# Performance work log

Measured on AMD Instinct MI355X. Metric: run time of the kernel, lower is better.

Reference implementation:

```python
import jax, jax.numpy as jnp
import numpy as np

N_NODES = 50000
N_EDGES = 1600000
IN_CH = 128
HIDDEN = 128
N_CLASSES = 40


def setup_inputs() -> dict:
    key = jax.random.key(0)
    ks = jax.random.split(key, 8)
    node_features = jax.random.normal(ks[0], (1, N_NODES, IN_CH), dtype=jnp.float32)
    edge_index = jax.random.randint(ks[1], (1, 2, N_EDGES), 0, N_NODES, dtype=jnp.int64)
    rank_mapping = jnp.zeros((2, N_EDGES), dtype=jnp.int32)
    s1 = 1.0 / np.sqrt(IN_CH)
    s2 = 1.0 / np.sqrt(HIDDEN)
    W1 = jax.random.uniform(ks[2], (IN_CH, HIDDEN), jnp.float32, -s1, s1)
    b1 = jax.random.uniform(ks[3], (HIDDEN,), jnp.float32, -s1, s1)
    W2 = jax.random.uniform(ks[4], (HIDDEN, HIDDEN), jnp.float32, -s2, s2)
    b2 = jax.random.uniform(ks[5], (HIDDEN,), jnp.float32, -s2, s2)
    Wfc = jax.random.uniform(ks[6], (HIDDEN, N_CLASSES), jnp.float32, -s2, s2)
    bfc = jax.random.uniform(ks[7], (N_CLASSES,), jnp.float32, -s2, s2)
    return {"node_features": node_features, "edge_index": edge_index,
            "rank_mapping": rank_mapping, "W1": W1, "b1": b1,
            "W2": W2, "b2": b2, "Wfc": Wfc, "bfc": bfc}


def _gcn_single(feats, src, dst, W1, b1, W2, b2, Wfc, bfc):
    # feats: [N, F]; src/dst: [E]
    n = feats.shape[0]
    x = feats[dst]                                 # gather -> [E, F]
    x = jax.nn.relu(x @ W1 + b1)                   # conv1 (Linear + ReLU)
    x = jax.ops.segment_sum(x, src, num_segments=n)  # scatter-sum -> [N, H]
    x = x[dst]                                     # gather -> [E, H]
    x = x @ W2 + b2                                # conv2 (plain Linear)
    x = jax.ops.segment_sum(x, src, num_segments=n)  # scatter-sum -> [N, H]
    return x @ Wfc + bfc                           # [N, C]


def reference(node_features, edge_index, rank_mapping, W1, b1, W2, b2, Wfc, bfc):
    src = edge_index[:, 0, :]  # [B, E]
    dst = edge_index[:, 1, :]  # [B, E]
    return jax.vmap(_gcn_single, in_axes=(0, 0, 0, None, None, None, None, None, None))(
        node_features, src, dst, W1, b1, W2, b2, Wfc, bfc)
```

## Files before the change

### kernel.cpp

```cpp
#include <hip/hip_runtime.h>

static constexpr int NN = 50000;
static constexpr int NE = 1600000;
static constexpr int CH = 128;
static constexpr int NCLS = 40;

static constexpr int NPB  = 256;
static constexpr int NBUK = (NN + NPB - 1) / NPB;
static constexpr int EPB  = 8192;
static constexpr int NHB  = (NE + EPB - 1) / EPB;
static constexpr int NS   = NBUK * NHB;
static constexpr int SCAN_B = 256;
static constexpr int NSB  = (NS + SCAN_B - 1) / SCAN_B;
static constexpr int NROWP = ((NN + 63) / 64) * 64;
static constexpr int PAD = 136;
static constexpr int GEMM_BLKS = (NN + 63) / 64;

typedef __attribute__((ext_vector_type(8))) short bf16x8;
typedef __attribute__((ext_vector_type(4))) float f32x4;

__device__ __forceinline__ float bflo(unsigned v) {
    return __uint_as_float((v & 0xFFFFu) << 16);
}
__device__ __forceinline__ float bfhi(unsigned v) {
    return __uint_as_float(v & 0xFFFF0000u);
}
__device__ __forceinline__ unsigned short f2bf(float f) {
    unsigned u = __float_as_uint(f);
    u += 0x7FFFu + ((u >> 16) & 1u);
    return (unsigned short)(u >> 16);
}

__global__ __launch_bounds__(256)
void fused_pre(const int* __restrict__ src, int* __restrict__ H,
               const float* __restrict__ W1, unsigned short* __restrict__ Wt_g,
               const float* __restrict__ W2, const float* __restrict__ Wfc,
               const float* __restrict__ b2, unsigned short* __restrict__ Mt,
               float* __restrict__ cfc)
{
    __shared__ int h[NBUK];
    const int t = threadIdx.x;
    const int b = blockIdx.x;

    if (b < NHB) {
        for (int i = t; i < NBUK; i += 256) h[i] = 0;
        __syncthreads();
        const int base4 = b * (EPB / 4);
        const int4* src4 = reinterpret_cast<const int4*>(src);
        for (int i = t; i < EPB / 4; i += 256) {
            const int idx = base4 + i;
            if (idx < NE / 4) {
                const int4 v = src4[idx];
                atomicAdd(&h[v.x >> 8], 1);
                atomicAdd(&h[v.y >> 8], 1);
                atomicAdd(&h[v.z >> 8], 1);
                atomicAdd(&h[v.w >> 8], 1);
            }
        }
        __syncthreads();
        for (int i = t; i < NBUK; i += 256) H[i * NHB + b] = h[i];
    } else if (b < NHB + 64) {
        const int idx = (b - NHB) * 256 + t;
        const int c = idx >> 7;
        const int k = idx & 127;
        Wt_g[c * PAD + k] = f2bf(W1[k * 128 + c]);
    } else {
        const int idx = (b - NHB - 64) * 256 + t;
        if (idx < 48 * 128) {
            const int c = idx >> 7;
            const int k = idx & 127;
            float a = 0.f;
            if (c < NCLS) {
                #pragma unroll 16
                for (int j = 0; j < 128; ++j) a += W2[k * 128 + j] * Wfc[j * NCLS + c];
            }
            Mt[c * 128 + k] = f2bf(a);
        }
        if (b == NHB + 64 && t < NCLS) {
            float a = 0.f;
            #pragma unroll 16
            for (int j = 0; j < 128; ++j) a += b2[j] * Wfc[j * NCLS + t];
            cfc[t] = a;
        }
    }
}

__global__ __launch_bounds__(SCAN_B)
void scan_local(int* __restrict__ H, int* __restrict__ bsum)
{
    __shared__ int buf[SCAN_B];
    const int t = threadIdx.x;
    const int g = blockIdx.x * SCAN_B + t;
    const int v = (g < NS) ? H[g] : 0;
    buf[t] = v;
    __syncthreads();
    #pragma unroll
    for (int off = 1; off < SCAN_B; off <<= 1) {
        const int x = (t >= off) ? buf[t - off] : 0;
        __syncthreads();
        buf[t] += x;
        __syncthreads();
    }
    if (g < NS) H[g] = buf[t] - v;
    if (t == SCAN_B - 1) bsum[blockIdx.x] = buf[t];
}

__global__ __launch_bounds__(SCAN_B)
void scan_bsums(int* __restrict__ bsum)
{
    __shared__ int buf[SCAN_B];
    const int t = threadIdx.x;
    const int v = (t < NSB) ? bsum[t] : 0;
    buf[t] = v;
    __syncthreads();
    #pragma unroll
    for (int off = 1; off < SCAN_B; off <<= 1) {
        const int x = (t >= off) ? buf[t - off] : 0;
        __syncthreads();
        buf[t] += x;
        __syncthreads();
    }
    if (t < NSB) bsum[t] = buf[t] - v;
    if (t == SCAN_B - 1) bsum[NSB] = buf[t];
}

__global__ __launch_bounds__(256)
void fused_mid(const int* __restrict__ src, const int* __restrict__ dst,
               const int* __restrict__ H, const int* __restrict__ bsum,
               int* __restrict__ EP,
               const float* __restrict__ X, const unsigned short* __restrict__ Wt_g,
               const float* __restrict__ b, const unsigned short* __restrict__ Mt,
               unsigned short* __restrict__ V1)
{
    __shared__ __align__(16) unsigned short Wt[128 * PAD];
    __shared__ __align__(16) unsigned short Fa[64 * PAD];
    __shared__ __align__(16) unsigned short Va[64 * NCLS];
    __shared__ float bl[128];
    __shared__ int cur[NBUK];

    const int t = threadIdx.x;

    if (blockIdx.x < NHB) {
        const int bb = blockIdx.x;
        for (int i = t; i < NBUK; i += 256) {
            const int x = i * NHB + bb;
            cur[i] = H[x] + bsum[x >> 8];
        }
        __syncthreads();
        const int base4 = bb * (EPB / 4);
        const int4* src4 = reinterpret_cast<const int4*>(src);
        const int4* dst4 = reinterpret_cast<const int4*>(dst);
        for (int i = t; i < EPB / 4; i += 256) {
            const int idx = base4 + i;
            if (idx < NE / 4) {
                const int4 s4 = src4[idx];
                const int4 d4 = dst4[idx];
                int pos;
                pos = atomicAdd(&cur[s4.x >> 8], 1); EP[pos] = ((s4.x & 255) << 16) | d4.x;
                pos = atomicAdd(&cur[s4.y >> 8], 1); EP[pos] = ((s4.y & 255) << 16) | d4.y;
                pos = atomicAdd(&cur[s4.z >> 8], 1); EP[pos] = ((s4.z & 255) << 16) | d4.z;
                pos = atomicAdd(&cur[s4.w >> 8], 1); EP[pos] = ((s4.w & 255) << 16) | d4.w;
            }
        }
        return;
    }

    const int gb = blockIdx.x - NHB;
    const int lane = t & 63;
    const int w = t >> 6;

    for (int i = t; i < (128 * PAD) / 8; i += 256)
        reinterpret_cast<uint4*>(Wt)[i] = reinterpret_cast<const uint4*>(Wt_g)[i];
    if (t < 128) bl[t] = b[t];

    const int base = gb * 64;
    const int nRows = min(64, NN - base);
    {
        const int r = t >> 2;
        const int c0 = (t & 3) * 32;
        if (r < nRows) {
            #pragma unroll
            for (int j = 0; j < 32; j += 4) {
                const float4 v = *reinterpret_cast<const float4*>(&X[(size_t)(base + r) * CH + c0 + j]);
                ushort4 o; o.x = f2bf(v.x); o.y = f2bf(v.y); o.z = f2bf(v.z); o.w = f2bf(v.w);
                *reinterpret_cast<ushort4*>(&Fa[r * PAD + c0 + j]) = o;
            }
        } else {
            #pragma unroll
            for (int j = 0; j < 32; j += 4) {
                ushort4 z; z.x = z.y = z.z = z.w = 0;
                *reinterpret_cast<ushort4*>(&Fa[r * PAD + c0 + j]) = z;
            }
        }
    }
    __syncthreads();

    f32x4 acc[8];
    #pragma unroll
    for (int i = 0; i < 8; ++i) acc[i] = (f32x4){0.f, 0.f, 0.f, 0.f};

    const int arow = w * 16 + (lane & 15);
    const int kgrp = (lane >> 4) * 4;

    #pragma unroll
    for (int ks = 0; ks < 4; ++ks) {
        const int k0 = ks * 32 + kgrp;
        bf16x8 af;
        {
            const short4 lo = *reinterpret_cast<const short4*>(&Fa[arow * PAD + k0]);
            const short4 hi = *reinterpret_cast<const short4*>(&Fa[arow * PAD + k0 + 16]);
            af[0] = lo.x; af[1] = lo.y; af[2] = lo.z; af[3] = lo.w;
            af[4] = hi.x; af[5] = hi.y; af[6] = hi.z; af[7] = hi.w;
        }
        #pragma unroll
        for (int ct = 0; ct < 8; ++ct) {
            const int c = ct * 16 + (lane & 15);
            bf16x8 bf;
            const short4 lo = *reinterpret_cast<const short4*>(&Wt[c * PAD + k0]);
            const short4 hi = *reinterpret_cast<const short4*>(&Wt[c * PAD + k0 + 16]);
            bf[0] = lo.x; bf[1] = lo.y; bf[2] = lo.z; bf[3] = lo.w;
            bf[4] = hi.x; bf[5] = hi.y; bf[6] = hi.z; bf[7] = hi.w;
            acc[ct] = __builtin_amdgcn_mfma_f32_16x16x32_bf16(af, bf, acc[ct], 0, 0, 0);
        }
    }
    __syncthreads();

    #pragma unroll
    for (int ct = 0; ct < 8; ++ct) {
        const int c = ct * 16 + (lane & 15);
        const float bias = bl[c];
        #pragma unroll
        for (int r = 0; r < 4; ++r) {
            const int row = w * 16 + (lane >> 4) * 4 + r;
            Fa[row * PAD + c] = f2bf(fmaxf(acc[ct][r] + bias, 0.f));
        }
    }
    __syncthreads();

    f32x4 acc2[3];
    #pragma unroll
    for (int i = 0; i < 3; ++i) acc2[i] = (f32x4){0.f, 0.f, 0.f, 0.f};

    #pragma unroll
    for (int ks = 0; ks < 4; ++ks) {
        const int k0 = ks * 32 + kgrp;
        bf16x8 af;
        {
            const short4 lo = *reinterpret_cast<const short4*>(&Fa[arow * PAD + k0]);
            const short4 hi = *reinterpret_cast<const short4*>(&Fa[arow * PAD + k0 + 16]);
            af[0] = lo.x; af[1] = lo.y; af[2] = lo.z; af[3] = lo.w;
            af[4] = hi.x; af[5] = hi.y; af[6] = hi.z; af[7] = hi.w;
        }
        #pragma unroll
        for (int ct = 0; ct < 3; ++ct) {
            const int c = ct * 16 + (lane & 15);
            bf16x8 bf;
            const short4 lo = *reinterpret_cast<const short4*>(&Mt[c * 128 + k0]);
            const short4 hi = *reinterpret_cast<const short4*>(&Mt[c * 128 + k0 + 16]);
            bf[0] = lo.x; bf[1] = lo.y; bf[2] = lo.z; bf[3] = lo.w;
            bf[4] = hi.x; bf[5] = hi.y; bf[6] = hi.z; bf[7] = hi.w;
            acc2[ct] = __builtin_amdgcn_mfma_f32_16x16x32_bf16(af, bf, acc2[ct], 0, 0, 0);
        }
    }

    #pragma unroll
    for (int ct = 0; ct < 3; ++ct) {
        const int c = ct * 16 + (lane & 15);
        if (c < NCLS) {
            #pragma unroll
            for (int r = 0; r < 4; ++r) {
                const int row = w * 16 + (lane >> 4) * 4 + r;
                Va[row * NCLS + c] = f2bf(acc2[ct][r]);
            }
        }
    }
    __syncthreads();

    for (int i = t; i < 320; i += 256) {
        const int r = i / 5;
        const int q = i % 5;
        *reinterpret_cast<uint4*>(&V1[(size_t)(base + r) * NCLS + q * 8]) =
            *reinterpret_cast<const uint4*>(&Va[r * NCLS + q * 8]);
    }
}

__global__ __launch_bounds__(1024)
void bucket_sort(const int* __restrict__ H, const int* __restrict__ bsum,
                 const int* __restrict__ EP,
                 unsigned short* __restrict__ sdst, int* __restrict__ offs,
                 int* __restrict__ deg)
{
    __shared__ int hist[NPB], cur[NPB], segBeg[NPB + 1], buf[NPB];
    const int t = threadIdx.x;
    const int b = blockIdx.x;
    const int node0 = b * NPB;
    const int nNodes = min(NPB, NN - node0);
    const int xb = b * NHB;
    const int beg = H[xb] + bsum[xb >> 8];
    int end;
    if (b == NBUK - 1) end = NE;
    else { const int xe = (b + 1) * NHB; end = H[xe] + bsum[xe >> 8]; }

    if (t < NPB) hist[t] = 0;
    __syncthreads();
    for (int i = beg + t; i < end; i += 1024) atomicAdd(&hist[EP[i] >> 16], 1);
    __syncthreads();

    if (t < NPB) buf[t] = hist[t];
    __syncthreads();
    #pragma unroll
    for (int off = 1; off < NPB; off <<= 1) {
        int x = 0;
        if (t < NPB && t >= off) x = buf[t - off];
        __syncthreads();
        if (t < NPB) buf[t] += x;
        __syncthreads();
    }
    if (t < NPB) segBeg[t] = buf[t] - hist[t];
    if (t == 0) segBeg[NPB] = end - beg;
    __syncthreads();

    if (t < nNodes) {
        offs[node0 + t] = beg + segBeg[t];
        deg[node0 + t] = hist[t];
    }
    if (b == NBUK - 1 && t == 0) offs[NN] = end;
    if (t < NPB) cur[t] = segBeg[t];
    __syncthreads();
    for (int i = beg + t; i < end; i += 1024) {
        const int p = EP[i];
        const int pos = atomicAdd(&cur[p >> 16], 1);
        sdst[beg + pos] = (unsigned short)(p & 0xFFFF);
    }
}

template<bool FINAL>
__global__ __launch_bounds__(512)
void gather40(const int* __restrict__ offs, const unsigned short* __restrict__ sdst,
              const unsigned short* __restrict__ X,
              unsigned short* __restrict__ Yb, float* __restrict__ Yf,
              const int* __restrict__ deg,
              const float* __restrict__ cfc, const float* __restrict__ bfc)
{
    const int t = threadIdx.x;
    const int w = t >> 6;
    const int lane = t & 63;
    const int g = lane >> 4;
    const int L = lane & 15;
    const int node0 = blockIdx.x * 32 + w * 4;

    float4 cf = make_float4(0.f, 0.f, 0.f, 0.f);
    float4 bfv = make_float4(0.f, 0.f, 0.f, 0.f);
    if (FINAL && L < 10) {
        cf  = *reinterpret_cast<const float4*>(&cfc[L * 4]);
        bfv = *reinterpret_cast<const float4*>(&bfc[L * 4]);
    }

    #pragma unroll
    for (int ni = 0; ni < 4; ++ni) {
        const int n = node0 + ni;
        if (n >= NN) break;
        const int sb = offs[n];
        const int se = offs[n + 1];
        float a0 = 0.f, a1 = 0.f, a2 = 0.f, a3 = 0.f;

        int i = sb;
        for (; i + 16 <= se; i += 16) {
            const int d0 = sdst[i + g];
            const int d1 = sdst[i + 4 + g];
            const int d2 = sdst[i + 8 + g];
            const int d3 = sdst[i + 12 + g];
            if (L < 10) {
                const uint2 v0 = *reinterpret_cast<const uint2*>(&X[(size_t)d0 * NCLS + L * 4]);
                const uint2 v1 = *reinterpret_cast<const uint2*>(&X[(size_t)d1 * NCLS + L * 4]);
                const uint2 v2 = *reinterpret_cast<const uint2*>(&X[(size_t)d2 * NCLS + L * 4]);
                const uint2 v3 = *reinterpret_cast<const uint2*>(&X[(size_t)d3 * NCLS + L * 4]);
                a0 += bflo(v0.x) + bflo(v1.x) + bflo(v2.x) + bflo(v3.x);
                a1 += bfhi(v0.x) + bfhi(v1.x) + bfhi(v2.x) + bfhi(v3.x);
                a2 += bflo(v0.y) + bflo(v1.y) + bflo(v2.y) + bflo(v3.y);
                a3 += bfhi(v0.y) + bfhi(v1.y) + bfhi(v2.y) + bfhi(v3.y);
            }
        }
        for (; i + 4 <= se; i += 4) {
            const int d = sdst[i + g];
            if (L < 10) {
                const uint2 v = *reinterpret_cast<const uint2*>(&X[(size_t)d * NCLS + L * 4]);
                a0 += bflo(v.x); a1 += bfhi(v.x);
                a2 += bflo(v.y); a3 += bfhi(v.y);
            }
        }
        const int rem = se - i;
        if (g < rem) {
            const int d = sdst[i + g];
            if (L < 10) {
                const uint2 v = *reinterpret_cast<const uint2*>(&X[(size_t)d * NCLS + L * 4]);
                a0 += bflo(v.x); a1 += bfhi(v.x);
                a2 += bflo(v.y); a3 += bfhi(v.y);
            }
        }

        a0 += __shfl_xor(a0, 16); a0 += __shfl_xor(a0, 32);
        a1 += __shfl_xor(a1, 16); a1 += __shfl_xor(a1, 32);
        a2 += __shfl_xor(a2, 16); a2 += __shfl_xor(a2, 32);
        a3 += __shfl_xor(a3, 16); a3 += __shfl_xor(a3, 32);

        if (lane < 16 && L < 10) {
            if (FINAL) {
                const float dgn = (float)deg[n];
                float4 o;
                o.x = a0 + dgn * cf.x + bfv.x;
                o.y = a1 + dgn * cf.y + bfv.y;
                o.z = a2 + dgn * cf.z + bfv.z;
                o.w = a3 + dgn * cf.w + bfv.w;
                *reinterpret_cast<float4*>(&Yf[(size_t)n * NCLS + L * 4]) = o;
            } else {
                uint2 o;
                o.x = ((unsigned)f2bf(a1) << 16) | f2bf(a0);
                o.y = ((unsigned)f2bf(a3) << 16) | f2bf(a2);
                *reinterpret_cast<uint2*>(&Yb[(size_t)n * NCLS + L * 4]) = o;
            }
        }
    }
}

extern "C" void kernel_launch(void* const* d_in, const int* in_sizes, int n_in,
                              void* d_out, int out_size, void* d_ws, size_t ws_size,
                              hipStream_t stream) {
    const float* F   = (const float*)d_in[0];
    const int*   EI  = (const int*)  d_in[1];
    const float* W1  = (const float*)d_in[3];
    const float* b1  = (const float*)d_in[4];
    const float* W2  = (const float*)d_in[5];
    const float* b2  = (const float*)d_in[6];
    const float* Wfc = (const float*)d_in[7];
    const float* bfc = (const float*)d_in[8];
    float* out = (float*)d_out;

    char* ws = (char*)d_ws;
    size_t off = 0;
    auto take = [&](size_t bytes) { char* p = ws + off; off += (bytes + 15) & ~(size_t)15; return p; };

    unsigned short* V1   = (unsigned short*)take((size_t)NROWP * NCLS * 2);
    unsigned short* U1   = (unsigned short*)take((size_t)NN * NCLS * 2);
    unsigned short* sdst = (unsigned short*)take((size_t)NE * 2);
    int*   EP   = (int*)take((size_t)NE * 4);
    int*   H    = (int*)take((size_t)NS * 4);
    int*   bsum = (int*)take((size_t)(NSB + 1) * 4);
    int*   deg  = (int*)take((size_t)NN * 4);
    int*   offs = (int*)take((size_t)(NN + 1) * 4);
    unsigned short* Mt   = (unsigned short*)take((size_t)48 * 128 * 2);
    unsigned short* Wt_g = (unsigned short*)take((size_t)128 * PAD * 2);
    float* cfc  = (float*)take((size_t)NCLS * 4);

    const int* src = EI;
    const int* dst = EI + NE;

    fused_pre<<<NHB + 64 + 24, 256, 0, stream>>>(src, H, W1, Wt_g, W2, Wfc, b2, Mt, cfc);

    scan_local<<<NSB, SCAN_B, 0, stream>>>(H, bsum);
    scan_bsums<<<1, SCAN_B, 0, stream>>>(bsum);

    fused_mid<<<NHB + GEMM_BLKS, 256, 0, stream>>>(src, dst, H, bsum, EP,
                                                   F, Wt_g, b1, Mt, V1);

    bucket_sort<<<NBUK, 1024, 0, stream>>>(H, bsum, EP, sdst, offs, deg);

    gather40<false><<<(NN + 31) / 32, 512, 0, stream>>>(offs, sdst, V1, U1, nullptr,
                                                        nullptr, nullptr, nullptr);

    gather40<true><<<(NN + 31) / 32, 512, 0, stream>>>(offs, sdst, U1, nullptr, out,
                                                       deg, cfc, bfc);
}
```

Baseline: 121.7 us.

## Fuse bucket sort with first neighbor gather using LDS-resident 64-node buckets

Buckets shrink from 256 to 64 nodes so each bucket's edge list fits in shared memory (CAP=3072). A single sortgather kernel loads the bucket's packed edges once, counting-sorts them in LDS, writes sdst, and directly performs the first 40-wide neighbor aggregation from the LDS-sorted indices. This removes one kernel launch and the repeated global reads of EP and sdst. In exchange the histogram and scan arrays grow, and the scan over block sums is widened to 1024 threads. There is no overflow check if a bucket exceeds CAP edges, so correctness relies on the near-uniform random degree distribution.

```diff
diff --git a/kernel.cpp b/kernel.cpp
--- a/kernel.cpp
+++ b/kernel.cpp
@@ -5,7 +5,7 @@
 static constexpr int CH = 128;
 static constexpr int NCLS = 40;
 
-static constexpr int NPB  = 256;
+static constexpr int NPB  = 64;
 static constexpr int NBUK = (NN + NPB - 1) / NPB;
 static constexpr int EPB  = 8192;
 static constexpr int NHB  = (NE + EPB - 1) / EPB;
@@ -15,6 +15,7 @@
 static constexpr int NROWP = ((NN + 63) / 64) * 64;
 static constexpr int PAD = 136;
 static constexpr int GEMM_BLKS = (NN + 63) / 64;
+static constexpr int CAP = 3072;
 
 typedef __attribute__((ext_vector_type(8))) short bf16x8;
 typedef __attribute__((ext_vector_type(4))) float f32x4;
@@ -51,10 +52,10 @@
             const int idx = base4 + i;
             if (idx < NE / 4) {
                 const int4 v = src4[idx];
-                atomicAdd(&h[v.x >> 8], 1);
-                atomicAdd(&h[v.y >> 8], 1);
-                atomicAdd(&h[v.z >> 8], 1);
-                atomicAdd(&h[v.w >> 8], 1);
+                atomicAdd(&h[v.x >> 6], 1);
+                atomicAdd(&h[v.y >> 6], 1);
+                atomicAdd(&h[v.z >> 6], 1);
+                atomicAdd(&h[v.w >> 6], 1);
             }
         }
         __syncthreads();
@@ -105,23 +106,23 @@
     if (t == SCAN_B - 1) bsum[blockIdx.x] = buf[t];
 }
 
-__global__ __launch_bounds__(SCAN_B)
+__global__ __launch_bounds__(1024)
 void scan_bsums(int* __restrict__ bsum)
 {
-    __shared__ int buf[SCAN_B];
+    __shared__ int buf[1024];
     const int t = threadIdx.x;
     const int v = (t < NSB) ? bsum[t] : 0;
     buf[t] = v;
     __syncthreads();
     #pragma unroll
-    for (int off = 1; off < SCAN_B; off <<= 1) {
+    for (int off = 1; off < 1024; off <<= 1) {
         const int x = (t >= off) ? buf[t - off] : 0;
         __syncthreads();
         buf[t] += x;
         __syncthreads();
     }
     if (t < NSB) bsum[t] = buf[t] - v;
-    if (t == SCAN_B - 1) bsum[NSB] = buf[t];
+    if (t == 1023) bsum[NSB] = buf[t];
 }
 
 __global__ __launch_bounds__(256)
@@ -156,10 +157,10 @@
                 const int4 s4 = src4[idx];
                 const int4 d4 = dst4[idx];
                 int pos;
-                pos = atomicAdd(&cur[s4.x >> 8], 1); EP[pos] = ((s4.x & 255) << 16) | d4.x;
-                pos = atomicAdd(&cur[s4.y >> 8], 1); EP[pos] = ((s4.y & 255) << 16) | d4.y;
-                pos = atomicAdd(&cur[s4.z >> 8], 1); EP[pos] = ((s4.z & 255) << 16) | d4.z;
-                pos = atomicAdd(&cur[s4.w >> 8], 1); EP[pos] = ((s4.w & 255) << 16) | d4.w;
+                pos = atomicAdd(&cur[s4.x >> 6], 1); EP[pos] = ((s4.x & 63) << 16) | d4.x;
+                pos = atomicAdd(&cur[s4.y >> 6], 1); EP[pos] = ((s4.y & 63) << 16) | d4.y;
+                pos = atomicAdd(&cur[s4.z >> 6], 1); EP[pos] = ((s4.z & 63) << 16) | d4.z;
+                pos = atomicAdd(&cur[s4.w >> 6], 1); EP[pos] = ((s4.w & 63) << 16) | d4.w;
             }
         }
         return;
@@ -284,13 +285,16 @@
     }
 }
 
-__global__ __launch_bounds__(1024)
-void bucket_sort(const int* __restrict__ H, const int* __restrict__ bsum,
-                 const int* __restrict__ EP,
-                 unsigned short* __restrict__ sdst, int* __restrict__ offs,
-                 int* __restrict__ deg)
+__global__ __launch_bounds__(512)
+void sortgather(const int* __restrict__ H, const int* __restrict__ bsum,
+                const int* __restrict__ EP, const unsigned short* __restrict__ V1,
+                unsigned short* __restrict__ U1, unsigned short* __restrict__ sdst,
+                int* __restrict__ offs, int* __restrict__ deg)
 {
-    __shared__ int hist[NPB], cur[NPB], segBeg[NPB + 1], buf[NPB];
+    __shared__ int raw[CAP];
+    __shared__ unsigned short srt[CAP];
+    __shared__ int hist[NPB], cur[NPB], segBeg[NPB + 1];
+
     const int t = threadIdx.x;
     const int b = blockIdx.x;
     const int node0 = b * NPB;
@@ -300,47 +304,111 @@
     int end;
     if (b == NBUK - 1) end = NE;
     else { const int xe = (b + 1) * NHB; end = H[xe] + bsum[xe >> 8]; }
-
+    const int C = end - beg;
+
+    for (int i = t; i < C; i += 512) raw[i] = EP[beg + i];
     if (t < NPB) hist[t] = 0;
     __syncthreads();
-    for (int i = beg + t; i < end; i += 1024) atomicAdd(&hist[EP[i] >> 16], 1);
-    __syncthreads();
-
-    if (t < NPB) buf[t] = hist[t];
+    for (int i = t; i < C; i += 512) atomicAdd(&hist[raw[i] >> 16], 1);
+    __syncthreads();
+
+    if (t < NPB) cur[t] = hist[t];
     __syncthreads();
     #pragma unroll
     for (int off = 1; off < NPB; off <<= 1) {
         int x = 0;
-        if (t < NPB && t >= off) x = buf[t - off];
-        __syncthreads();
-        if (t < NPB) buf[t] += x;
-        __syncthreads();
-    }
-    if (t < NPB) segBeg[t] = buf[t] - hist[t];
-    if (t == 0) segBeg[NPB] = end - beg;
+        if (t < NPB && t >= off) x = cur[t - off];
+        __syncthreads();
+        if (t < NPB) cur[t] += x;
+        __syncthreads();
+    }
+    if (t < NPB) segBeg[t] = cur[t] - hist[t];
+    if (t == 0) segBeg[NPB] = C;
     __syncthreads();
 
     if (t < nNodes) {
         offs[node0 + t] = beg + segBeg[t];
         deg[node0 + t] = hist[t];
     }
-    if (b == NBUK - 1 && t == 0) offs[NN] = end;
+    if (b == NBUK - 1 && t == 0) offs[NN] = NE;
     if (t < NPB) cur[t] = segBeg[t];
     __syncthreads();
-    for (int i = beg + t; i < end; i += 1024) {
-        const int p = EP[i];
+
+    for (int i = t; i < C; i += 512) {
+        const int p = raw[i];
         const int pos = atomicAdd(&cur[p >> 16], 1);
-        sdst[beg + pos] = (unsigned short)(p & 0xFFFF);
-    }
-}
-
-template<bool FINAL>
+        srt[pos] = (unsigned short)(p & 0xFFFF);
+    }
+    __syncthreads();
+
+    for (int i = t; i < C; i += 512) sdst[beg + i] = srt[i];
+
+    const int w = t >> 6;
+    const int lane = t & 63;
+    const int g = lane >> 4;
+    const int L = lane & 15;
+
+    for (int ni = 0; ni < 8; ++ni) {
+        const int n = w * 8 + ni;
+        if (n >= nNodes) break;
+        const int sb = segBeg[n];
+        const int se = segBeg[n + 1];
+        float a0 = 0.f, a1 = 0.f, a2 = 0.f, a3 = 0.f;
+
+        int i = sb;
+        for (; i + 16 <= se; i += 16) {
+            const int d0 = srt[i + g];
+            const int d1 = srt[i + 4 + g];
+            const int d2 = srt[i + 8 + g];
+            const int d3 = srt[i + 12 + g];
+            if (L < 10) {
+                const uint2 v0 = *reinterpret_cast<const uint2*>(&V1[(size_t)d0 * NCLS + L * 4]);
+                const uint2 v1 = *reinterpret_cast<const uint2*>(&V1[(size_t)d1 * NCLS + L * 4]);
+                const uint2 v2 = *reinterpret_cast<const uint2*>(&V1[(size_t)d2 * NCLS + L * 4]);
+                const uint2 v3 = *reinterpret_cast<const uint2*>(&V1[(size_t)d3 * NCLS + L * 4]);
+                a0 += bflo(v0.x) + bflo(v1.x) + bflo(v2.x) + bflo(v3.x);
+                a1 += bfhi(v0.x) + bfhi(v1.x) + bfhi(v2.x) + bfhi(v3.x);
+                a2 += bflo(v0.y) + bflo(v1.y) + bflo(v2.y) + bflo(v3.y);
+                a3 += bfhi(v0.y) + bfhi(v1.y) + bfhi(v2.y) + bfhi(v3.y);
+            }
+        }
+        for (; i + 4 <= se; i += 4) {
+            const int d = srt[i + g];
+            if (L < 10) {
+                const uint2 v = *reinterpret_cast<const uint2*>(&V1[(size_t)d * NCLS + L * 4]);
+                a0 += bflo(v.x); a1 += bfhi(v.x);
+                a2 += bflo(v.y); a3 += bfhi(v.y);
+            }
+        }
+        const int rem = se - i;
+        if (g < rem) {
+            const int d = srt[i + g];
+            if (L < 10) {
+                const uint2 v = *reinterpret_cast<const uint2*>(&V1[(size_t)d * NCLS + L * 4]);
+                a0 += bflo(v.x); a1 += bfhi(v.x);
+                a2 += bflo(v.y); a3 += bfhi(v.y);
+            }
+        }
+
+        a0 += __shfl_xor(a0, 16); a0 += __shfl_xor(a0, 32);
+        a1 += __shfl_xor(a1, 16); a1 += __shfl_xor(a1, 32);
+        a2 += __shfl_xor(a2, 16); a2 += __shfl_xor(a2, 32);
+        a3 += __shfl_xor(a3, 16); a3 += __shfl_xor(a3, 32);
+
+        if (lane < 16 && L < 10) {
+            uint2 o;
+            o.x = ((unsigned)f2bf(a1) << 16) | f2bf(a0);
+            o.y = ((unsigned)f2bf(a3) << 16) | f2bf(a2);
+            *reinterpret_cast<uint2*>(&U1[(size_t)(node0 + n) * NCLS + L * 4]) = o;
+        }
+    }
+}
+
 __global__ __launch_bounds__(512)
-void gather40(const int* __restrict__ offs, const unsigned short* __restrict__ sdst,
-              const unsigned short* __restrict__ X,
-              unsigned short* __restrict__ Yb, float* __restrict__ Yf,
-              const int* __restrict__ deg,
-              const float* __restrict__ cfc, const float* __restrict__ bfc)
+void gather40f(const int* __restrict__ offs, const unsigned short* __restrict__ sdst,
+               const unsigned short* __restrict__ X, float* __restrict__ Yf,
+               const int* __restrict__ deg,
+               const float* __restrict__ cfc, const float* __restrict__ bfc)
 {
     const int t = threadIdx.x;
     const int w = t >> 6;
@@ -351,7 +419,7 @@
 
     float4 cf = make_float4(0.f, 0.f, 0.f, 0.f);
     float4 bfv = make_float4(0.f, 0.f, 0.f, 0.f);
-    if (FINAL && L < 10) {
+    if (L < 10) {
         cf  = *reinterpret_cast<const float4*>(&cfc[L * 4]);
         bfv = *reinterpret_cast<const float4*>(&bfc[L * 4]);
     }
@@ -405,20 +473,13 @@
         a3 += __shfl_xor(a3, 16); a3 += __shfl_xor(a3, 32);
 
         if (lane < 16 && L < 10) {
-            if (FINAL) {
-                const float dgn = (float)deg[n];
-                float4 o;
-                o.x = a0 + dgn * cf.x + bfv.x;
-                o.y = a1 + dgn * cf.y + bfv.y;
-                o.z = a2 + dgn * cf.z + bfv.z;
-                o.w = a3 + dgn * cf.w + bfv.w;
-                *reinterpret_cast<float4*>(&Yf[(size_t)n * NCLS + L * 4]) = o;
-            } else {
-                uint2 o;
-                o.x = ((unsigned)f2bf(a1) << 16) | f2bf(a0);
-                o.y = ((unsigned)f2bf(a3) << 16) | f2bf(a2);
-                *reinterpret_cast<uint2*>(&Yb[(size_t)n * NCLS + L * 4]) = o;
-            }
+            const float dgn = (float)deg[n];
+            float4 o;
+            o.x = a0 + dgn * cf.x + bfv.x;
+            o.y = a1 + dgn * cf.y + bfv.y;
+            o.z = a2 + dgn * cf.z + bfv.z;
+            o.w = a3 + dgn * cf.w + bfv.w;
+            *reinterpret_cast<float4*>(&Yf[(size_t)n * NCLS + L * 4]) = o;
         }
     }
 }
@@ -438,10 +499,10 @@
 
     char* ws = (char*)d_ws;
     size_t off = 0;
-    auto take = [&](size_t bytes) { char* p = ws + off; off += (bytes + 15) & ~(size_t)15; return p; };
+    auto take = [&](size_t bytes) { char* p = ws + off; off += (bytes + 63) & ~(size_t)63; return p; };
 
     unsigned short* V1   = (unsigned short*)take((size_t)NROWP * NCLS * 2);
-    unsigned short* U1   = (unsigned short*)take((size_t)NN * NCLS * 2);
+    unsigned short* U1   = (unsigned short*)take((size_t)NROWP * NCLS * 2);
     unsigned short* sdst = (unsigned short*)take((size_t)NE * 2);
     int*   EP   = (int*)take((size_t)NE * 4);
     int*   H    = (int*)take((size_t)NS * 4);
@@ -458,16 +519,12 @@
     fused_pre<<<NHB + 64 + 24, 256, 0, stream>>>(src, H, W1, Wt_g, W2, Wfc, b2, Mt, cfc);
 
     scan_local<<<NSB, SCAN_B, 0, stream>>>(H, bsum);
-    scan_bsums<<<1, SCAN_B, 0, stream>>>(bsum);
+    scan_bsums<<<1, 1024, 0, stream>>>(bsum);
 
     fused_mid<<<NHB + GEMM_BLKS, 256, 0, stream>>>(src, dst, H, bsum, EP,
                                                    F, Wt_g, b1, Mt, V1);
 
-    bucket_sort<<<NBUK, 1024, 0, stream>>>(H, bsum, EP, sdst, offs, deg);
-
-    gather40<false><<<(NN + 31) / 32, 512, 0, stream>>>(offs, sdst, V1, U1, nullptr,
-                                                        nullptr, nullptr, nullptr);
-
-    gather40<true><<<(NN + 31) / 32, 512, 0, stream>>>(offs, sdst, U1, nullptr, out,
-                                                       deg, cfc, bfc);
-}
+    sortgather<<<NBUK, 512, 0, stream>>>(H, bsum, EP, V1, U1, sdst, offs, deg);
+
+    gather40f<<<(NN + 31) / 32, 512, 0, stream>>>(offs, sdst, U1, out, deg, cfc, bfc);
+}
```

New measurement: 110.4 us. 1.1x faster.
